# Performance work log

Measured on AMD Instinct MI355X. Metric: run time of the kernel, lower is better.

Reference implementation:

```python
import jax, jax.numpy as jnp
import numpy as np

N_NODES = 100000
N_EDGES = 1600000
NUM_FEATS = 128
HIDDEN = 16
NUM_CLASSES = 40


def setup_inputs() -> dict:
    key = jax.random.key(0)
    k1, k2, k3, k4, k5 = jax.random.split(key, 5)
    x = jax.random.normal(k1, (N_NODES, NUM_FEATS), dtype=jnp.float32)
    edge_weight = jax.random.uniform(k2, (N_EDGES,), dtype=jnp.float32)
    # Glorot-uniform linear weights (bias=False in the module)
    lim1 = float(np.sqrt(6.0 / (NUM_FEATS + HIDDEN)))
    lim2 = float(np.sqrt(6.0 / (HIDDEN + NUM_CLASSES)))
    W1 = jax.random.uniform(k3, (NUM_FEATS, HIDDEN), dtype=jnp.float32, minval=-lim1, maxval=lim1)
    W2 = jax.random.uniform(k4, (HIDDEN, NUM_CLASSES), dtype=jnp.float32, minval=-lim2, maxval=lim2)
    edge_index = jax.random.randint(k5, (2, N_EDGES), 0, N_NODES, dtype=jnp.int64)
    return {"x": x, "edge_weight": edge_weight, "W1": W1, "W2": W2, "edge_index": edge_index}


def _sgconv(h, W, src, dst, edge_weight, n):
    # SGConv (K=1): weighted neighbor aggregation + self loop (weight 1), then bias-free linear
    msg = edge_weight[:, None] * h[src]                      # [E, d] gather + scale
    agg = jax.ops.segment_sum(msg, dst, num_segments=n) + h  # scatter-add + self loop
    return agg @ W


def reference(x, edge_weight, W1, W2, edge_index):
    src, dst = edge_index[0], edge_index[1]
    n = x.shape[0]
    h = _sgconv(x, W1, src, dst, edge_weight, n)   # [N, 16]
    # dropout(p=0.5) is identity in eval mode
    h = _sgconv(h, W2, src, dst, edge_weight, n)   # [N, num_classes]
    return jax.nn.log_softmax(h, axis=1)
```

## Files before the change

### kernel.cpp

```cpp
#include <hip/hip_runtime.h>

#define NFEAT 128
#define HID 16
#define NCLS 40
#define BSHIFT 7
#define BNODES 128
#define CAP 2560
#define NBUCK_MAX 800
#define BIN_CHUNK 4096
#define APAD 17

#define SCALE1 262144.0f
#define SCALE2 65536.0f

typedef __attribute__((ext_vector_type(8))) short short8;
typedef __attribute__((ext_vector_type(4))) float f32x4;

__device__ __forceinline__ unsigned bf16_rne(float f) {
    unsigned u = __float_as_uint(f);
    return (u + 0x7FFFu + ((u >> 16) & 1u)) >> 16;
}
__device__ __forceinline__ float bf_lo(unsigned u) { return __uint_as_float(u << 16); }
__device__ __forceinline__ float bf_hi(unsigned u) { return __uint_as_float(u & 0xFFFF0000u); }

__global__ __launch_bounds__(256) void zero_kernel(int* __restrict__ p, int m)
{
    int i = blockIdx.x * 256 + threadIdx.x;
    if (i < m) p[i] = 0;
}

__global__ __launch_bounds__(256) void bin_kernel(const int* __restrict__ src,
                                                  const int* __restrict__ dst,
                                                  const float* __restrict__ ew,
                                                  int* __restrict__ cursor,
                                                  int2* __restrict__ slab,
                                                  int E, int nbuck)
{
    __shared__ int hist[NBUCK_MAX];
    __shared__ int runbase[NBUCK_MAX];
    __shared__ int lbase[NBUCK_MAX];
    __shared__ int2 ebuf[BIN_CHUNK];
    __shared__ unsigned short sbuck[BIN_CHUNK];
    __shared__ int sTotal;
    int tid = threadIdx.x;
    for (int i = tid; i < NBUCK_MAX; i += 256) hist[i] = 0;
    __syncthreads();

    int base = blockIdx.x * BIN_CHUNK;
    int myd[16], mys[16], myw[16];
    #pragma unroll
    for (int k = 0; k < 16; ++k) {
        int e = base + k * 256 + tid;
        if (e < E) {
            myd[k] = dst[e];
            mys[k] = src[e];
            myw[k] = __float_as_int(ew[e]);
            atomicAdd(&hist[myd[k] >> BSHIFT], 1);
        } else myd[k] = -1;
    }
    __syncthreads();

    for (int i = tid; i < nbuck; i += 256) {
        int c = hist[i];
        if (c) runbase[i] = i * CAP + atomicAdd(&cursor[i], c);
    }
    if (tid < 64) {
        int lane = tid;
        int carry = 0;
        for (int i0 = 0; i0 < NBUCK_MAX; i0 += 64) {
            int i = i0 + lane;
            int v = (i < NBUCK_MAX) ? hist[i] : 0;
            int incl = v;
            #pragma unroll
            for (int off = 1; off < 64; off <<= 1) {
                int t = __shfl_up(incl, off);
                if (lane >= off) incl += t;
            }
            if (i < NBUCK_MAX) lbase[i] = carry + incl - v;
            carry += __shfl(incl, 63);
        }
        if (lane == 0) sTotal = carry;
    }
    __syncthreads();

    for (int i = tid; i < NBUCK_MAX; i += 256) hist[i] = 0;
    __syncthreads();
    #pragma unroll
    for (int k = 0; k < 16; ++k) {
        int d = myd[k];
        if (d >= 0) {
            int b = d >> BSHIFT;
            int r = atomicAdd(&hist[b], 1);
            int j = lbase[b] + r;
            ebuf[j]  = make_int2(mys[k] | ((d & (BNODES - 1)) << 20), myw[k]);
            sbuck[j] = (unsigned short)b;
        }
    }
    __syncthreads();

    int totalv = sTotal;
    for (int j = tid; j < totalv; j += 256) {
        int b = sbuck[j];
        int pos = runbase[b] + (j - lbase[b]);
        if (pos < (b + 1) * CAP)
            slab[pos] = ebuf[j];
    }
}

__global__ __launch_bounds__(256) void gemm1_mfma_kernel(const float* __restrict__ x,
                                                         const float* __restrict__ W1,
                                                         unsigned short* __restrict__ h1b,
                                                         int n)
{
    int tid  = threadIdx.x;
    int wave = tid >> 6, lane = tid & 63;
    int m = lane & 15, q = lane >> 4;
    int base = blockIdx.x * 64 + wave * 16;

    short8 bfrag[4];
    #pragma unroll
    for (int kc = 0; kc < 4; ++kc) {
        #pragma unroll
        for (int j = 0; j < 8; ++j)
            bfrag[kc][j] = (short)bf16_rne(W1[(kc * 32 + q * 8 + j) * HID + m]);
    }

    int rowa = base + m; if (rowa > n - 1) rowa = n - 1;
    const float* xr = x + (size_t)rowa * NFEAT;
    f32x4 acc = {0.f, 0.f, 0.f, 0.f};
    #pragma unroll
    for (int kc = 0; kc < 4; ++kc) {
        float4 a0 = *(const float4*)(xr + kc * 32 + q * 8);
        float4 a1 = *(const float4*)(xr + kc * 32 + q * 8 + 4);
        short8 af;
        af[0] = (short)bf16_rne(a0.x); af[1] = (short)bf16_rne(a0.y);
        af[2] = (short)bf16_rne(a0.z); af[3] = (short)bf16_rne(a0.w);
        af[4] = (short)bf16_rne(a1.x); af[5] = (short)bf16_rne(a1.y);
        af[6] = (short)bf16_rne(a1.z); af[7] = (short)bf16_rne(a1.w);
        acc = __builtin_amdgcn_mfma_f32_16x16x32_bf16(af, bfrag[kc], acc, 0, 0, 0);
    }
    #pragma unroll
    for (int reg = 0; reg < 4; ++reg) {
        int rowd = base + q * 4 + reg;
        if (rowd < n)
            h1b[(size_t)rowd * HID + m] = (unsigned short)bf16_rne(acc[reg]);
    }
}

__global__ __launch_bounds__(512) void gather1_kernel(const uint4* __restrict__ hq,
                                                      const int* __restrict__ cursor,
                                                      const int2* __restrict__ slab,
                                                      uint4* __restrict__ outb, int n)
{
    __shared__ int accum[BNODES * APAD];
    int tid = threadIdx.x;
    #pragma unroll
    for (int i = tid; i < BNODES * APAD; i += 512) accum[i] = 0;
    __syncthreads();

    int b = blockIdx.x;
    int beg = b * CAP;
    int cnt = cursor[b]; if (cnt > CAP) cnt = CAP;
    int total = cnt * 2;

    int i0 = tid, i1 = tid + 512;
    int2 e0, e1; uint4 q0;
    if (i0 < total) e0 = slab[beg + (i0 >> 1)];
    if (i1 < total) e1 = slab[beg + (i1 >> 1)];
    if (i0 < total) q0 = hq[(size_t)(e0.x & 0xFFFFF) * 2 + (i0 & 1)];

    while (i0 < total) {
        uint4 q1;
        if (i1 < total) q1 = hq[(size_t)(e1.x & 0xFFFFF) * 2 + (i1 & 1)];
        int i2 = i1 + 512;
        int2 e2;
        if (i2 < total) e2 = slab[beg + (i2 >> 1)];

        int p  = i0 & 1;
        int dl = (e0.x >> 20) & (BNODES - 1);
        float wsc = __int_as_float(e0.y) * SCALE1;
        int* a = &accum[dl * APAD + p * 8];
        atomicAdd(a + 0, __float2int_rn(wsc * bf_lo(q0.x)));
        atomicAdd(a + 1, __float2int_rn(wsc * bf_hi(q0.x)));
        atomicAdd(a + 2, __float2int_rn(wsc * bf_lo(q0.y)));
        atomicAdd(a + 3, __float2int_rn(wsc * bf_hi(q0.y)));
        atomicAdd(a + 4, __float2int_rn(wsc * bf_lo(q0.z)));
        atomicAdd(a + 5, __float2int_rn(wsc * bf_hi(q0.z)));
        atomicAdd(a + 6, __float2int_rn(wsc * bf_lo(q0.w)));
        atomicAdd(a + 7, __float2int_rn(wsc * bf_hi(q0.w)));

        e0 = e1; e1 = e2; q0 = q1; i0 = i1; i1 = i2;
    }
    __syncthreads();

    const float inv = 1.0f / SCALE1;
    if (tid < BNODES * 2) {
        int dl = tid >> 1, p = tid & 1;
        int node = (b << BSHIFT) + dl;
        if (node < n) {
            uint4 qs = hq[(size_t)node * 2 + p];
            const int* a = &accum[dl * APAD + p * 8];
            uint4 o;
            o.x = bf16_rne((float)a[0] * inv + bf_lo(qs.x)) |
                  (bf16_rne((float)a[1] * inv + bf_hi(qs.x)) << 16);
            o.y = bf16_rne((float)a[2] * inv + bf_lo(qs.y)) |
                  (bf16_rne((float)a[3] * inv + bf_hi(qs.y)) << 16);
            o.z = bf16_rne((float)a[4] * inv + bf_lo(qs.z)) |
                  (bf16_rne((float)a[5] * inv + bf_hi(qs.z)) << 16);
            o.w = bf16_rne((float)a[6] * inv + bf_lo(qs.w)) |
                  (bf16_rne((float)a[7] * inv + bf_hi(qs.w)) << 16);
            outb[(size_t)node * 2 + p] = o;
        }
    }
}

#define ZPAD 41
__global__ __launch_bounds__(512) void gather2_lsm_kernel(const uint4* __restrict__ hq,
                                                          const int* __restrict__ cursor,
                                                          const int2* __restrict__ slab,
                                                          const float* __restrict__ W2,
                                                          float* __restrict__ out, int n)
{
    __shared__ int   accum[BNODES * APAD];
    __shared__ float w2s[HID * NCLS];
    __shared__ float zbuf[BNODES * ZPAD];
    int tid = threadIdx.x;
    #pragma unroll
    for (int i = tid; i < BNODES * APAD; i += 512) accum[i] = 0;
    for (int i = tid; i < HID * NCLS; i += 512) w2s[i] = W2[i];
    __syncthreads();

    int b = blockIdx.x;
    int beg = b * CAP;
    int cnt = cursor[b]; if (cnt > CAP) cnt = CAP;
    int node0 = b << BSHIFT;
    int total = cnt * 2;

    int i0 = tid, i1 = tid + 512;
    int2 e0, e1; uint4 q0;
    if (i0 < total) e0 = slab[beg + (i0 >> 1)];
    if (i1 < total) e1 = slab[beg + (i1 >> 1)];
    if (i0 < total) q0 = hq[(size_t)(e0.x & 0xFFFFF) * 2 + (i0 & 1)];

    while (i0 < total) {
        uint4 q1;
        if (i1 < total) q1 = hq[(size_t)(e1.x & 0xFFFFF) * 2 + (i1 & 1)];
        int i2 = i1 + 512;
        int2 e2;
        if (i2 < total) e2 = slab[beg + (i2 >> 1)];

        int p  = i0 & 1;
        int dl = (e0.x >> 20) & (BNODES - 1);
        float wsc = __int_as_float(e0.y) * SCALE2;
        int* a = &accum[dl * APAD + p * 8];
        atomicAdd(a + 0, __float2int_rn(wsc * bf_lo(q0.x)));
        atomicAdd(a + 1, __float2int_rn(wsc * bf_hi(q0.x)));
        atomicAdd(a + 2, __float2int_rn(wsc * bf_lo(q0.y)));
        atomicAdd(a + 3, __float2int_rn(wsc * bf_hi(q0.y)));
        atomicAdd(a + 4, __float2int_rn(wsc * bf_lo(q0.z)));
        atomicAdd(a + 5, __float2int_rn(wsc * bf_hi(q0.z)));
        atomicAdd(a + 6, __float2int_rn(wsc * bf_lo(q0.w)));
        atomicAdd(a + 7, __float2int_rn(wsc * bf_hi(q0.w)));

        e0 = e1; e1 = e2; q0 = q1; i0 = i1; i1 = i2;
    }
    __syncthreads();

    const float inv = 1.0f / SCALE2;
    if (tid < BNODES) {
        int dl = tid;
        int node = node0 + dl;
        if (node < n) {
            uint4 qa = hq[(size_t)node * 2 + 0];
            uint4 qb = hq[(size_t)node * 2 + 1];
            float r[HID];
            const int* a = &accum[dl * APAD];
            r[0]  = (float)a[ 0] * inv + bf_lo(qa.x);
            r[1]  = (float)a[ 1] * inv + bf_hi(qa.x);
            r[2]  = (float)a[ 2] * inv + bf_lo(qa.y);
            r[3]  = (float)a[ 3] * inv + bf_hi(qa.y);
            r[4]  = (float)a[ 4] * inv + bf_lo(qa.z);
            r[5]  = (float)a[ 5] * inv + bf_hi(qa.z);
            r[6]  = (float)a[ 6] * inv + bf_lo(qa.w);
            r[7]  = (float)a[ 7] * inv + bf_hi(qa.w);
            r[8]  = (float)a[ 8] * inv + bf_lo(qb.x);
            r[9]  = (float)a[ 9] * inv + bf_hi(qb.x);
            r[10] = (float)a[10] * inv + bf_lo(qb.y);
            r[11] = (float)a[11] * inv + bf_hi(qb.y);
            r[12] = (float)a[12] * inv + bf_lo(qb.z);
            r[13] = (float)a[13] * inv + bf_hi(qb.z);
            r[14] = (float)a[14] * inv + bf_lo(qb.w);
            r[15] = (float)a[15] * inv + bf_hi(qb.w);

            float z[NCLS];
            #pragma unroll
            for (int j = 0; j < NCLS; ++j) z[j] = 0.f;
            #pragma unroll
            for (int f = 0; f < HID; ++f) {
                float rf = r[f];
                #pragma unroll
                for (int j = 0; j < NCLS; ++j)
                    z[j] += rf * w2s[f * NCLS + j];
            }
            float m = z[0];
            #pragma unroll
            for (int j = 1; j < NCLS; ++j) m = fmaxf(m, z[j]);
            float ssum = 0.f;
            #pragma unroll
            for (int j = 0; j < NCLS; ++j) ssum += __expf(z[j] - m);
            float l = m + __logf(ssum);
            #pragma unroll
            for (int j = 0; j < NCLS; ++j) zbuf[dl * ZPAD + j] = z[j] - l;
        }
    }
    __syncthreads();

    for (int i = tid; i < BNODES * NCLS; i += 512) {
        int nl = i / NCLS, j = i - nl * NCLS;
        if (node0 + nl < n)
            out[(size_t)node0 * NCLS + i] = zbuf[nl * ZPAD + j];
    }
}

extern "C" void kernel_launch(void* const* d_in, const int* in_sizes, int n_in,
                              void* d_out, int out_size, void* d_ws, size_t ws_size,
                              hipStream_t stream)
{
    const float* x  = (const float*)d_in[0];
    const float* ew = (const float*)d_in[1];
    const float* W1 = (const float*)d_in[2];
    const float* W2 = (const float*)d_in[3];
    const int*   ei = (const int*)d_in[4];

    int n = in_sizes[0] / NFEAT;
    int E = in_sizes[1];
    const int* src = ei;
    const int* dst = ei + E;
    float* out = (float*)d_out;

    int nbuck = (n + BNODES - 1) >> BSHIFT;
    int nbin  = (E + BIN_CHUNK - 1) / BIN_CHUNK;

    char* w = (char*)d_ws;
    int*  cursor = (int*)w;  w += NBUCK_MAX * 4;
    w = (char*)(((size_t)w + 15) & ~(size_t)15);
    int2* slab   = (int2*)w; w += (size_t)NBUCK_MAX * CAP * 8;
    unsigned short* h1b = (unsigned short*)w; w += (size_t)n * HID * 2;
    unsigned short* h2b = (unsigned short*)w; w += (size_t)n * HID * 2;

    zero_kernel<<<(NBUCK_MAX + 255) / 256, 256, 0, stream>>>(cursor, NBUCK_MAX);
    bin_kernel<<<nbin, 256, 0, stream>>>(src, dst, ew, cursor, slab, E, nbuck);
    gemm1_mfma_kernel<<<(n + 63) / 64, 256, 0, stream>>>(x, W1, h1b, n);
    gather1_kernel<<<nbuck, 512, 0, stream>>>((const uint4*)h1b, cursor, slab,
                                              (uint4*)h2b, n);
    gather2_lsm_kernel<<<nbuck, 512, 0, stream>>>((const uint4*)h2b, cursor, slab,
                                                  W2, out, n);
}
```

Before: 171.9 us.

## Fuse whole pipeline into one cooperative persistent kernel with grid syncs

Replaces the five separate launches (zero, bin, gemm, gather1, gather2+log_softmax) with a single cooperative kernel of 256 persistent blocks that uses grid-wide syncs between phases. Binning and the first GEMM become one shared work queue, and binning now scatters straight to the slab without the local staging buffer or prefix scan. The aim is to remove launch gaps and tail effects between kernels. In exchange there are grid-sync costs, only 256 blocks covering about 800 buckets per gather phase, and less coalesced slab writes. If the cooperative launch fails, it falls back to a multi-kernel path that also fuses bin and GEMM.

```diff
diff --git a/kernel.cpp b/kernel.cpp
--- a/kernel.cpp
+++ b/kernel.cpp
@@ -1,4 +1,7 @@
 #include <hip/hip_runtime.h>
+#include <hip/hip_cooperative_groups.h>
+
+namespace cg = cooperative_groups;
 
 #define NFEAT 128
 #define HID 16
@@ -9,6 +12,7 @@
 #define NBUCK_MAX 800
 #define BIN_CHUNK 4096
 #define APAD 17
+#define ZPAD 41
 
 #define SCALE1 262144.0f
 #define SCALE2 65536.0f
@@ -22,6 +26,267 @@
 }
 __device__ __forceinline__ float bf_lo(unsigned u) { return __uint_as_float(u << 16); }
 __device__ __forceinline__ float bf_hi(unsigned u) { return __uint_as_float(u & 0xFFFF0000u); }
+
+__global__ __launch_bounds__(512, 2) void mega_kernel(
+    const int* __restrict__ src, const int* __restrict__ dst,
+    const float* __restrict__ ew, int* __restrict__ cursor,
+    int2* __restrict__ slab, int E, int nbuck, int nbin,
+    const float* __restrict__ x, const float* __restrict__ W1,
+    unsigned short* __restrict__ h1b, unsigned short* __restrict__ h2b,
+    const float* __restrict__ W2, float* __restrict__ out, int n)
+{
+    __shared__ int   hist[NBUCK_MAX];
+    __shared__ int   runbase[NBUCK_MAX];
+    __shared__ int   accum[BNODES * APAD];
+    __shared__ float w2s[HID * NCLS];
+    __shared__ float zbuf[BNODES * ZPAD];
+
+    cg::grid_group grid = cg::this_grid();
+    const int tid = threadIdx.x;
+    const int bid = blockIdx.x;
+    const int G   = gridDim.x;
+
+    for (int i = bid * 512 + tid; i < NBUCK_MAX; i += G * 512) cursor[i] = 0;
+    grid.sync();
+
+    int ngemm = (n + 127) >> 7;
+    int nunits = nbin + ngemm;
+    for (int u = bid; u < nunits; u += G) {
+        if (u < nbin) {
+            for (int i = tid; i < NBUCK_MAX; i += 512) hist[i] = 0;
+            __syncthreads();
+            int base = u * BIN_CHUNK;
+            int myd[8], mys[8], myw[8];
+            #pragma unroll
+            for (int k = 0; k < 8; ++k) {
+                int e = base + k * 512 + tid;
+                if (e < E) {
+                    myd[k] = dst[e];
+                    mys[k] = src[e];
+                    myw[k] = __float_as_int(ew[e]);
+                    atomicAdd(&hist[myd[k] >> BSHIFT], 1);
+                } else myd[k] = -1;
+            }
+            __syncthreads();
+            for (int i = tid; i < nbuck; i += 512) {
+                int c = hist[i];
+                runbase[i] = c ? (i * CAP + atomicAdd(&cursor[i], c)) : 0;
+                hist[i] = 0;
+            }
+            __syncthreads();
+            #pragma unroll
+            for (int k = 0; k < 8; ++k) {
+                int d = myd[k];
+                if (d >= 0) {
+                    int b = d >> BSHIFT;
+                    int pos = runbase[b] + atomicAdd(&hist[b], 1);
+                    if (pos < (b + 1) * CAP)
+                        slab[pos] = make_int2(mys[k] | ((d & (BNODES - 1)) << 20), myw[k]);
+                }
+            }
+            __syncthreads();
+        } else {
+            int wave = tid >> 6, lane = tid & 63;
+            int m = lane & 15, q = lane >> 4;
+            int rbase = (u - nbin) * 128 + wave * 16;
+
+            short8 bfrag[4];
+            #pragma unroll
+            for (int kc = 0; kc < 4; ++kc) {
+                #pragma unroll
+                for (int j = 0; j < 8; ++j)
+                    bfrag[kc][j] = (short)bf16_rne(W1[(kc * 32 + q * 8 + j) * HID + m]);
+            }
+            int rowa = rbase + m; if (rowa > n - 1) rowa = n - 1;
+            const float* xr = x + (size_t)rowa * NFEAT;
+            f32x4 acc = {0.f, 0.f, 0.f, 0.f};
+            #pragma unroll
+            for (int kc = 0; kc < 4; ++kc) {
+                float4 a0 = *(const float4*)(xr + kc * 32 + q * 8);
+                float4 a1 = *(const float4*)(xr + kc * 32 + q * 8 + 4);
+                short8 af;
+                af[0] = (short)bf16_rne(a0.x); af[1] = (short)bf16_rne(a0.y);
+                af[2] = (short)bf16_rne(a0.z); af[3] = (short)bf16_rne(a0.w);
+                af[4] = (short)bf16_rne(a1.x); af[5] = (short)bf16_rne(a1.y);
+                af[6] = (short)bf16_rne(a1.z); af[7] = (short)bf16_rne(a1.w);
+                acc = __builtin_amdgcn_mfma_f32_16x16x32_bf16(af, bfrag[kc], acc, 0, 0, 0);
+            }
+            #pragma unroll
+            for (int reg = 0; reg < 4; ++reg) {
+                int rowd = rbase + q * 4 + reg;
+                if (rowd < n)
+                    h1b[(size_t)rowd * HID + m] = (unsigned short)bf16_rne(acc[reg]);
+            }
+        }
+    }
+    grid.sync();
+
+    {
+        const uint4* hq = (const uint4*)h1b;
+        uint4* outb = (uint4*)h2b;
+        for (int b = bid; b < nbuck; b += G) {
+            for (int i = tid; i < BNODES * APAD; i += 512) accum[i] = 0;
+            __syncthreads();
+
+            int beg = b * CAP;
+            int cnt = cursor[b]; if (cnt > CAP) cnt = CAP;
+            int total = cnt * 2;
+
+            int i0 = tid, i1 = tid + 512;
+            int2 e0, e1; uint4 q0;
+            if (i0 < total) e0 = slab[beg + (i0 >> 1)];
+            if (i1 < total) e1 = slab[beg + (i1 >> 1)];
+            if (i0 < total) q0 = hq[(size_t)(e0.x & 0xFFFFF) * 2 + (i0 & 1)];
+
+            while (i0 < total) {
+                uint4 q1;
+                if (i1 < total) q1 = hq[(size_t)(e1.x & 0xFFFFF) * 2 + (i1 & 1)];
+                int i2 = i1 + 512;
+                int2 e2;
+                if (i2 < total) e2 = slab[beg + (i2 >> 1)];
+
+                int p  = i0 & 1;
+                int dl = (e0.x >> 20) & (BNODES - 1);
+                float wsc = __int_as_float(e0.y) * SCALE1;
+                int* a = &accum[dl * APAD + p * 8];
+                atomicAdd(a + 0, __float2int_rn(wsc * bf_lo(q0.x)));
+                atomicAdd(a + 1, __float2int_rn(wsc * bf_hi(q0.x)));
+                atomicAdd(a + 2, __float2int_rn(wsc * bf_lo(q0.y)));
+                atomicAdd(a + 3, __float2int_rn(wsc * bf_hi(q0.y)));
+                atomicAdd(a + 4, __float2int_rn(wsc * bf_lo(q0.z)));
+                atomicAdd(a + 5, __float2int_rn(wsc * bf_hi(q0.z)));
+                atomicAdd(a + 6, __float2int_rn(wsc * bf_lo(q0.w)));
+                atomicAdd(a + 7, __float2int_rn(wsc * bf_hi(q0.w)));
+
+                e0 = e1; e1 = e2; q0 = q1; i0 = i1; i1 = i2;
+            }
+            __syncthreads();
+
+            const float inv = 1.0f / SCALE1;
+            if (tid < BNODES * 2) {
+                int dl = tid >> 1, p = tid & 1;
+                int node = (b << BSHIFT) + dl;
+                if (node < n) {
+                    uint4 qs = hq[(size_t)node * 2 + p];
+                    const int* a = &accum[dl * APAD + p * 8];
+                    uint4 o;
+                    o.x = bf16_rne((float)a[0] * inv + bf_lo(qs.x)) |
+                          (bf16_rne((float)a[1] * inv + bf_hi(qs.x)) << 16);
+                    o.y = bf16_rne((float)a[2] * inv + bf_lo(qs.y)) |
+                          (bf16_rne((float)a[3] * inv + bf_hi(qs.y)) << 16);
+                    o.z = bf16_rne((float)a[4] * inv + bf_lo(qs.z)) |
+                          (bf16_rne((float)a[5] * inv + bf_hi(qs.z)) << 16);
+                    o.w = bf16_rne((float)a[6] * inv + bf_lo(qs.w)) |
+                          (bf16_rne((float)a[7] * inv + bf_hi(qs.w)) << 16);
+                    outb[(size_t)node * 2 + p] = o;
+                }
+            }
+            __syncthreads();
+        }
+    }
+    grid.sync();
+
+    {
+        const uint4* hq = (const uint4*)h2b;
+        for (int i = tid; i < HID * NCLS; i += 512) w2s[i] = W2[i];
+        for (int b = bid; b < nbuck; b += G) {
+            for (int i = tid; i < BNODES * APAD; i += 512) accum[i] = 0;
+            __syncthreads();
+
+            int beg = b * CAP;
+            int cnt = cursor[b]; if (cnt > CAP) cnt = CAP;
+            int node0 = b << BSHIFT;
+            int total = cnt * 2;
+
+            int i0 = tid, i1 = tid + 512;
+            int2 e0, e1; uint4 q0;
+            if (i0 < total) e0 = slab[beg + (i0 >> 1)];
+            if (i1 < total) e1 = slab[beg + (i1 >> 1)];
+            if (i0 < total) q0 = hq[(size_t)(e0.x & 0xFFFFF) * 2 + (i0 & 1)];
+
+            while (i0 < total) {
+                uint4 q1;
+                if (i1 < total) q1 = hq[(size_t)(e1.x & 0xFFFFF) * 2 + (i1 & 1)];
+                int i2 = i1 + 512;
+                int2 e2;
+                if (i2 < total) e2 = slab[beg + (i2 >> 1)];
+
+                int p  = i0 & 1;
+                int dl = (e0.x >> 20) & (BNODES - 1);
+                float wsc = __int_as_float(e0.y) * SCALE2;
+                int* a = &accum[dl * APAD + p * 8];
+                atomicAdd(a + 0, __float2int_rn(wsc * bf_lo(q0.x)));
+                atomicAdd(a + 1, __float2int_rn(wsc * bf_hi(q0.x)));
+                atomicAdd(a + 2, __float2int_rn(wsc * bf_lo(q0.y)));
+                atomicAdd(a + 3, __float2int_rn(wsc * bf_hi(q0.y)));
+                atomicAdd(a + 4, __float2int_rn(wsc * bf_lo(q0.z)));
+                atomicAdd(a + 5, __float2int_rn(wsc * bf_hi(q0.z)));
+                atomicAdd(a + 6, __float2int_rn(wsc * bf_lo(q0.w)));
+                atomicAdd(a + 7, __float2int_rn(wsc * bf_hi(q0.w)));
+
+                e0 = e1; e1 = e2; q0 = q1; i0 = i1; i1 = i2;
+            }
+            __syncthreads();
+
+            const float inv = 1.0f / SCALE2;
+            if (tid < BNODES) {
+                int dl = tid;
+                int node = node0 + dl;
+                if (node < n) {
+                    uint4 qa = hq[(size_t)node * 2 + 0];
+                    uint4 qb = hq[(size_t)node * 2 + 1];
+                    float r[HID];
+                    const int* a = &accum[dl * APAD];
+                    r[0]  = (float)a[ 0] * inv + bf_lo(qa.x);
+                    r[1]  = (float)a[ 1] * inv + bf_hi(qa.x);
+                    r[2]  = (float)a[ 2] * inv + bf_lo(qa.y);
+                    r[3]  = (float)a[ 3] * inv + bf_hi(qa.y);
+                    r[4]  = (float)a[ 4] * inv + bf_lo(qa.z);
+                    r[5]  = (float)a[ 5] * inv + bf_hi(qa.z);
+                    r[6]  = (float)a[ 6] * inv + bf_lo(qa.w);
+                    r[7]  = (float)a[ 7] * inv + bf_hi(qa.w);
+                    r[8]  = (float)a[ 8] * inv + bf_lo(qb.x);
+                    r[9]  = (float)a[ 9] * inv + bf_hi(qb.x);
+                    r[10] = (float)a[10] * inv + bf_lo(qb.y);
+                    r[11] = (float)a[11] * inv + bf_hi(qb.y);
+                    r[12] = (float)a[12] * inv + bf_lo(qb.z);
+                    r[13] = (float)a[13] * inv + bf_hi(qb.z);
+                    r[14] = (float)a[14] * inv + bf_lo(qb.w);
+                    r[15] = (float)a[15] * inv + bf_hi(qb.w);
+
+                    float z[NCLS];
+                    #pragma unroll
+                    for (int j = 0; j < NCLS; ++j) z[j] = 0.f;
+                    #pragma unroll
+                    for (int f = 0; f < HID; ++f) {
+                        float rf = r[f];
+                        #pragma unroll
+                        for (int j = 0; j < NCLS; ++j)
+                            z[j] += rf * w2s[f * NCLS + j];
+                    }
+                    float m = z[0];
+                    #pragma unroll
+                    for (int j = 1; j < NCLS; ++j) m = fmaxf(m, z[j]);
+                    float ssum = 0.f;
+                    #pragma unroll
+                    for (int j = 0; j < NCLS; ++j) ssum += __expf(z[j] - m);
+                    float l = m + __logf(ssum);
+                    #pragma unroll
+                    for (int j = 0; j < NCLS; ++j) zbuf[dl * ZPAD + j] = z[j] - l;
+                }
+            }
+            __syncthreads();
+
+            for (int i = tid; i < BNODES * NCLS; i += 512) {
+                int nl = i / NCLS, j = i - nl * NCLS;
+                if (node0 + nl < n)
+                    out[(size_t)node0 * NCLS + i] = zbuf[nl * ZPAD + j];
+            }
+            __syncthreads();
+        }
+    }
+}
+
 
 __global__ __launch_bounds__(256) void zero_kernel(int* __restrict__ p, int m)
 {
@@ -29,121 +294,87 @@
     if (i < m) p[i] = 0;
 }
 
-__global__ __launch_bounds__(256) void bin_kernel(const int* __restrict__ src,
-                                                  const int* __restrict__ dst,
-                                                  const float* __restrict__ ew,
-                                                  int* __restrict__ cursor,
-                                                  int2* __restrict__ slab,
-                                                  int E, int nbuck)
+__global__ __launch_bounds__(256) void bin_gemm_kernel(const int* __restrict__ src,
+                                                       const int* __restrict__ dst,
+                                                       const float* __restrict__ ew,
+                                                       int* __restrict__ cursor,
+                                                       int2* __restrict__ slab,
+                                                       int E, int nbuck, int nbin,
+                                                       const float* __restrict__ x,
+                                                       const float* __restrict__ W1,
+                                                       unsigned short* __restrict__ h1b,
+                                                       int n)
 {
     __shared__ int hist[NBUCK_MAX];
     __shared__ int runbase[NBUCK_MAX];
-    __shared__ int lbase[NBUCK_MAX];
-    __shared__ int2 ebuf[BIN_CHUNK];
-    __shared__ unsigned short sbuck[BIN_CHUNK];
-    __shared__ int sTotal;
     int tid = threadIdx.x;
-    for (int i = tid; i < NBUCK_MAX; i += 256) hist[i] = 0;
-    __syncthreads();
-
-    int base = blockIdx.x * BIN_CHUNK;
-    int myd[16], mys[16], myw[16];
-    #pragma unroll
-    for (int k = 0; k < 16; ++k) {
-        int e = base + k * 256 + tid;
-        if (e < E) {
-            myd[k] = dst[e];
-            mys[k] = src[e];
-            myw[k] = __float_as_int(ew[e]);
-            atomicAdd(&hist[myd[k] >> BSHIFT], 1);
-        } else myd[k] = -1;
-    }
-    __syncthreads();
-
-    for (int i = tid; i < nbuck; i += 256) {
-        int c = hist[i];
-        if (c) runbase[i] = i * CAP + atomicAdd(&cursor[i], c);
-    }
-    if (tid < 64) {
-        int lane = tid;
-        int carry = 0;
-        for (int i0 = 0; i0 < NBUCK_MAX; i0 += 64) {
-            int i = i0 + lane;
-            int v = (i < NBUCK_MAX) ? hist[i] : 0;
-            int incl = v;
-            #pragma unroll
-            for (int off = 1; off < 64; off <<= 1) {
-                int t = __shfl_up(incl, off);
-                if (lane >= off) incl += t;
-            }
-            if (i < NBUCK_MAX) lbase[i] = carry + incl - v;
-            carry += __shfl(incl, 63);
-        }
-        if (lane == 0) sTotal = carry;
-    }
-    __syncthreads();
-
-    for (int i = tid; i < NBUCK_MAX; i += 256) hist[i] = 0;
-    __syncthreads();
-    #pragma unroll
-    for (int k = 0; k < 16; ++k) {
-        int d = myd[k];
-        if (d >= 0) {
-            int b = d >> BSHIFT;
-            int r = atomicAdd(&hist[b], 1);
-            int j = lbase[b] + r;
-            ebuf[j]  = make_int2(mys[k] | ((d & (BNODES - 1)) << 20), myw[k]);
-            sbuck[j] = (unsigned short)b;
-        }
-    }
-    __syncthreads();
-
-    int totalv = sTotal;
-    for (int j = tid; j < totalv; j += 256) {
-        int b = sbuck[j];
-        int pos = runbase[b] + (j - lbase[b]);
-        if (pos < (b + 1) * CAP)
-            slab[pos] = ebuf[j];
-    }
-}
-
-__global__ __launch_bounds__(256) void gemm1_mfma_kernel(const float* __restrict__ x,
-                                                         const float* __restrict__ W1,
-                                                         unsigned short* __restrict__ h1b,
-                                                         int n)
-{
-    int tid  = threadIdx.x;
-    int wave = tid >> 6, lane = tid & 63;
-    int m = lane & 15, q = lane >> 4;
-    int base = blockIdx.x * 64 + wave * 16;
-
-    short8 bfrag[4];
-    #pragma unroll
-    for (int kc = 0; kc < 4; ++kc) {
+
+    if (blockIdx.x < nbin) {
+        for (int i = tid; i < NBUCK_MAX; i += 256) hist[i] = 0;
+        __syncthreads();
+
+        int base = blockIdx.x * BIN_CHUNK;
+        int myd[16], mys[16], myw[16];
         #pragma unroll
-        for (int j = 0; j < 8; ++j)
-            bfrag[kc][j] = (short)bf16_rne(W1[(kc * 32 + q * 8 + j) * HID + m]);
-    }
-
-    int rowa = base + m; if (rowa > n - 1) rowa = n - 1;
-    const float* xr = x + (size_t)rowa * NFEAT;
-    f32x4 acc = {0.f, 0.f, 0.f, 0.f};
-    #pragma unroll
-    for (int kc = 0; kc < 4; ++kc) {
-        float4 a0 = *(const float4*)(xr + kc * 32 + q * 8);
-        float4 a1 = *(const float4*)(xr + kc * 32 + q * 8 + 4);
-        short8 af;
-        af[0] = (short)bf16_rne(a0.x); af[1] = (short)bf16_rne(a0.y);
-        af[2] = (short)bf16_rne(a0.z); af[3] = (short)bf16_rne(a0.w);
-        af[4] = (short)bf16_rne(a1.x); af[5] = (short)bf16_rne(a1.y);
-        af[6] = (short)bf16_rne(a1.z); af[7] = (short)bf16_rne(a1.w);
-        acc = __builtin_amdgcn_mfma_f32_16x16x32_bf16(af, bfrag[kc], acc, 0, 0, 0);
-    }
-    #pragma unroll
-    for (int reg = 0; reg < 4; ++reg) {
-        int rowd = base + q * 4 + reg;
-        if (rowd < n)
-            h1b[(size_t)rowd * HID + m] = (unsigned short)bf16_rne(acc[reg]);
+        for (int k = 0; k < 16; ++k) {
+            int e = base + k * 256 + tid;
+            if (e < E) {
+                myd[k] = dst[e];
+                mys[k] = src[e];
+                myw[k] = __float_as_int(ew[e]);
+                atomicAdd(&hist[myd[k] >> BSHIFT], 1);
+            } else myd[k] = -1;
+        }
+        __syncthreads();
+        for (int i = tid; i < nbuck; i += 256) {
+            int c = hist[i];
+            runbase[i] = c ? (i * CAP + atomicAdd(&cursor[i], c)) : 0;
+            hist[i] = 0;
+        }
+        __syncthreads();
+        #pragma unroll
+        for (int k = 0; k < 16; ++k) {
+            int d = myd[k];
+            if (d >= 0) {
+                int b = d >> BSHIFT;
+                int pos = runbase[b] + atomicAdd(&hist[b], 1);
+                if (pos < (b + 1) * CAP)
+                    slab[pos] = make_int2(mys[k] | ((d & (BNODES - 1)) << 20), myw[k]);
+            }
+        }
+    } else {
+        int wave = tid >> 6, lane = tid & 63;
+        int m = lane & 15, q = lane >> 4;
+        int base = (blockIdx.x - nbin) * 64 + wave * 16;
+
+        short8 bfrag[4];
+        #pragma unroll
+        for (int kc = 0; kc < 4; ++kc) {
+            #pragma unroll
+            for (int j = 0; j < 8; ++j)
+                bfrag[kc][j] = (short)bf16_rne(W1[(kc * 32 + q * 8 + j) * HID + m]);
+        }
+
+        int rowa = base + m; if (rowa > n - 1) rowa = n - 1;
+        const float* xr = x + (size_t)rowa * NFEAT;
+        f32x4 acc = {0.f, 0.f, 0.f, 0.f};
+        #pragma unroll
+        for (int kc = 0; kc < 4; ++kc) {
+            float4 a0 = *(const float4*)(xr + kc * 32 + q * 8);
+            float4 a1 = *(const float4*)(xr + kc * 32 + q * 8 + 4);
+            short8 af;
+            af[0] = (short)bf16_rne(a0.x); af[1] = (short)bf16_rne(a0.y);
+            af[2] = (short)bf16_rne(a0.z); af[3] = (short)bf16_rne(a0.w);
+            af[4] = (short)bf16_rne(a1.x); af[5] = (short)bf16_rne(a1.y);
+            af[6] = (short)bf16_rne(a1.z); af[7] = (short)bf16_rne(a1.w);
+            acc = __builtin_amdgcn_mfma_f32_16x16x32_bf16(af, bfrag[kc], acc, 0, 0, 0);
+        }
+        #pragma unroll
+        for (int reg = 0; reg < 4; ++reg) {
+            int rowd = base + q * 4 + reg;
+            if (rowd < n)
+                h1b[(size_t)rowd * HID + m] = (unsigned short)bf16_rne(acc[reg]);
+        }
     }
 }
 
@@ -214,7 +445,6 @@
     }
 }
 
-#define ZPAD 41
 __global__ __launch_bounds__(512) void gather2_lsm_kernel(const uint4* __restrict__ hq,
                                                           const int* __restrict__ cursor,
                                                           const int2* __restrict__ slab,
@@ -348,11 +578,21 @@
     unsigned short* h1b = (unsigned short*)w; w += (size_t)n * HID * 2;
     unsigned short* h2b = (unsigned short*)w; w += (size_t)n * HID * 2;
 
-    zero_kernel<<<(NBUCK_MAX + 255) / 256, 256, 0, stream>>>(cursor, NBUCK_MAX);
-    bin_kernel<<<nbin, 256, 0, stream>>>(src, dst, ew, cursor, slab, E, nbuck);
-    gemm1_mfma_kernel<<<(n + 63) / 64, 256, 0, stream>>>(x, W1, h1b, n);
-    gather1_kernel<<<nbuck, 512, 0, stream>>>((const uint4*)h1b, cursor, slab,
-                                              (uint4*)h2b, n);
-    gather2_lsm_kernel<<<nbuck, 512, 0, stream>>>((const uint4*)h2b, cursor, slab,
-                                                  W2, out, n);
-}
+    void* kargs[] = {
+        (void*)&src, (void*)&dst, (void*)&ew, (void*)&cursor, (void*)&slab,
+        (void*)&E, (void*)&nbuck, (void*)&nbin, (void*)&x, (void*)&W1,
+        (void*)&h1b, (void*)&h2b, (void*)&W2, (void*)&out, (void*)&n
+    };
+    hipError_t err = hipLaunchCooperativeKernel((void*)mega_kernel, dim3(256),
+                                                dim3(512), kargs, 0, stream);
+    if (err != hipSuccess) {
+        int ngemm64 = (n + 63) / 64;
+        zero_kernel<<<(NBUCK_MAX + 255) / 256, 256, 0, stream>>>(cursor, NBUCK_MAX);
+        bin_gemm_kernel<<<nbin + ngemm64, 256, 0, stream>>>(src, dst, ew, cursor, slab,
+                                                            E, nbuck, nbin, x, W1, h1b, n);
+        gather1_kernel<<<nbuck, 512, 0, stream>>>((const uint4*)h1b, cursor, slab,
+                                                  (uint4*)h2b, n);
+        gather2_lsm_kernel<<<nbuck, 512, 0, stream>>>((const uint4*)h2b, cursor, slab,
+                                                      W2, out, n);
+    }
+}
```

After: 268.0 us. +55.9%, slower.

## Merge binning and GEMM1 into one launch, deepen gather prefetch pipelines

Applied to the files above, without the earlier changes.

Binning and the first MFMA GEMM now run as disjoint block ranges of a single kernel, so the two independent stages overlap and one launch is saved. The binning path drops the LDS staging buffer and prefix scan and scatters each edge straight to its global slab slot. This reduces LDS use, which may raise occupancy, but the global writes are less coalesced. Both gather kernels prefetch four edges and three feature rows ahead instead of two and one, and carry occupancy hints in their launch bounds, trading registers for more memory-level parallelism.

```diff
diff --git a/kernel.cpp b/kernel.cpp
--- a/kernel.cpp
+++ b/kernel.cpp
@@ -9,6 +9,7 @@
 #define NBUCK_MAX 800
 #define BIN_CHUNK 4096
 #define APAD 17
+#define ZPAD 41
 
 #define SCALE1 262144.0f
 #define SCALE2 65536.0f
@@ -29,128 +30,94 @@
     if (i < m) p[i] = 0;
 }
 
-__global__ __launch_bounds__(256) void bin_kernel(const int* __restrict__ src,
-                                                  const int* __restrict__ dst,
-                                                  const float* __restrict__ ew,
-                                                  int* __restrict__ cursor,
-                                                  int2* __restrict__ slab,
-                                                  int E, int nbuck)
+__global__ __launch_bounds__(256) void bin_gemm_kernel(const int* __restrict__ src,
+                                                       const int* __restrict__ dst,
+                                                       const float* __restrict__ ew,
+                                                       int* __restrict__ cursor,
+                                                       int2* __restrict__ slab,
+                                                       int E, int nbuck, int nbin,
+                                                       const float* __restrict__ x,
+                                                       const float* __restrict__ W1,
+                                                       unsigned short* __restrict__ h1b,
+                                                       int n)
 {
     __shared__ int hist[NBUCK_MAX];
     __shared__ int runbase[NBUCK_MAX];
-    __shared__ int lbase[NBUCK_MAX];
-    __shared__ int2 ebuf[BIN_CHUNK];
-    __shared__ unsigned short sbuck[BIN_CHUNK];
-    __shared__ int sTotal;
     int tid = threadIdx.x;
-    for (int i = tid; i < NBUCK_MAX; i += 256) hist[i] = 0;
-    __syncthreads();
-
-    int base = blockIdx.x * BIN_CHUNK;
-    int myd[16], mys[16], myw[16];
-    #pragma unroll
-    for (int k = 0; k < 16; ++k) {
-        int e = base + k * 256 + tid;
-        if (e < E) {
-            myd[k] = dst[e];
-            mys[k] = src[e];
-            myw[k] = __float_as_int(ew[e]);
-            atomicAdd(&hist[myd[k] >> BSHIFT], 1);
-        } else myd[k] = -1;
-    }
-    __syncthreads();
-
-    for (int i = tid; i < nbuck; i += 256) {
-        int c = hist[i];
-        if (c) runbase[i] = i * CAP + atomicAdd(&cursor[i], c);
-    }
-    if (tid < 64) {
-        int lane = tid;
-        int carry = 0;
-        for (int i0 = 0; i0 < NBUCK_MAX; i0 += 64) {
-            int i = i0 + lane;
-            int v = (i < NBUCK_MAX) ? hist[i] : 0;
-            int incl = v;
-            #pragma unroll
-            for (int off = 1; off < 64; off <<= 1) {
-                int t = __shfl_up(incl, off);
-                if (lane >= off) incl += t;
+
+    if (blockIdx.x < nbin) {
+        for (int i = tid; i < NBUCK_MAX; i += 256) hist[i] = 0;
+        __syncthreads();
+
+        int base = blockIdx.x * BIN_CHUNK;
+        int myd[16], mys[16], myw[16];
+        #pragma unroll
+        for (int k = 0; k < 16; ++k) {
+            int e = base + k * 256 + tid;
+            if (e < E) {
+                myd[k] = dst[e];
+                mys[k] = src[e];
+                myw[k] = __float_as_int(ew[e]);
+                atomicAdd(&hist[myd[k] >> BSHIFT], 1);
+            } else myd[k] = -1;
+        }
+        __syncthreads();
+        for (int i = tid; i < nbuck; i += 256) {
+            int c = hist[i];
+            runbase[i] = c ? (i * CAP + atomicAdd(&cursor[i], c)) : 0;
+            hist[i] = 0;
+        }
+        __syncthreads();
+        #pragma unroll
+        for (int k = 0; k < 16; ++k) {
+            int d = myd[k];
+            if (d >= 0) {
+                int b = d >> BSHIFT;
+                int pos = runbase[b] + atomicAdd(&hist[b], 1);
+                if (pos < (b + 1) * CAP)
+                    slab[pos] = make_int2(mys[k] | ((d & (BNODES - 1)) << 20), myw[k]);
             }
-            if (i < NBUCK_MAX) lbase[i] = carry + incl - v;
-            carry += __shfl(incl, 63);
-        }
-        if (lane == 0) sTotal = carry;
-    }
-    __syncthreads();
-
-    for (int i = tid; i < NBUCK_MAX; i += 256) hist[i] = 0;
-    __syncthreads();
-    #pragma unroll
-    for (int k = 0; k < 16; ++k) {
-        int d = myd[k];
-        if (d >= 0) {
-            int b = d >> BSHIFT;
-            int r = atomicAdd(&hist[b], 1);
-            int j = lbase[b] + r;
-            ebuf[j]  = make_int2(mys[k] | ((d & (BNODES - 1)) << 20), myw[k]);
-            sbuck[j] = (unsigned short)b;
-        }
-    }
-    __syncthreads();
-
-    int totalv = sTotal;
-    for (int j = tid; j < totalv; j += 256) {
-        int b = sbuck[j];
-        int pos = runbase[b] + (j - lbase[b]);
-        if (pos < (b + 1) * CAP)
-            slab[pos] = ebuf[j];
-    }
-}
-
-__global__ __launch_bounds__(256) void gemm1_mfma_kernel(const float* __restrict__ x,
-                                                         const float* __restrict__ W1,
-                                                         unsigned short* __restrict__ h1b,
-                                                         int n)
-{
-    int tid  = threadIdx.x;
-    int wave = tid >> 6, lane = tid & 63;
-    int m = lane & 15, q = lane >> 4;
-    int base = blockIdx.x * 64 + wave * 16;
-
-    short8 bfrag[4];
-    #pragma unroll
-    for (int kc = 0; kc < 4; ++kc) {
-        #pragma unroll
-        for (int j = 0; j < 8; ++j)
-            bfrag[kc][j] = (short)bf16_rne(W1[(kc * 32 + q * 8 + j) * HID + m]);
-    }
-
-    int rowa = base + m; if (rowa > n - 1) rowa = n - 1;
-    const float* xr = x + (size_t)rowa * NFEAT;
-    f32x4 acc = {0.f, 0.f, 0.f, 0.f};
-    #pragma unroll
-    for (int kc = 0; kc < 4; ++kc) {
-        float4 a0 = *(const float4*)(xr + kc * 32 + q * 8);
-        float4 a1 = *(const float4*)(xr + kc * 32 + q * 8 + 4);
-        short8 af;
-        af[0] = (short)bf16_rne(a0.x); af[1] = (short)bf16_rne(a0.y);
-        af[2] = (short)bf16_rne(a0.z); af[3] = (short)bf16_rne(a0.w);
-        af[4] = (short)bf16_rne(a1.x); af[5] = (short)bf16_rne(a1.y);
-        af[6] = (short)bf16_rne(a1.z); af[7] = (short)bf16_rne(a1.w);
-        acc = __builtin_amdgcn_mfma_f32_16x16x32_bf16(af, bfrag[kc], acc, 0, 0, 0);
-    }
-    #pragma unroll
-    for (int reg = 0; reg < 4; ++reg) {
-        int rowd = base + q * 4 + reg;
-        if (rowd < n)
-            h1b[(size_t)rowd * HID + m] = (unsigned short)bf16_rne(acc[reg]);
-    }
-}
-
-__global__ __launch_bounds__(512) void gather1_kernel(const uint4* __restrict__ hq,
-                                                      const int* __restrict__ cursor,
-                                                      const int2* __restrict__ slab,
-                                                      uint4* __restrict__ outb, int n)
+        }
+    } else {
+        int wave = tid >> 6, lane = tid & 63;
+        int m = lane & 15, q = lane >> 4;
+        int base = (blockIdx.x - nbin) * 64 + wave * 16;
+
+        short8 bfrag[4];
+        #pragma unroll
+        for (int kc = 0; kc < 4; ++kc) {
+            #pragma unroll
+            for (int j = 0; j < 8; ++j)
+                bfrag[kc][j] = (short)bf16_rne(W1[(kc * 32 + q * 8 + j) * HID + m]);
+        }
+
+        int rowa = base + m; if (rowa > n - 1) rowa = n - 1;
+        const float* xr = x + (size_t)rowa * NFEAT;
+        f32x4 acc = {0.f, 0.f, 0.f, 0.f};
+        #pragma unroll
+        for (int kc = 0; kc < 4; ++kc) {
+            float4 a0 = *(const float4*)(xr + kc * 32 + q * 8);
+            float4 a1 = *(const float4*)(xr + kc * 32 + q * 8 + 4);
+            short8 af;
+            af[0] = (short)bf16_rne(a0.x); af[1] = (short)bf16_rne(a0.y);
+            af[2] = (short)bf16_rne(a0.z); af[3] = (short)bf16_rne(a0.w);
+            af[4] = (short)bf16_rne(a1.x); af[5] = (short)bf16_rne(a1.y);
+            af[6] = (short)bf16_rne(a1.z); af[7] = (short)bf16_rne(a1.w);
+            acc = __builtin_amdgcn_mfma_f32_16x16x32_bf16(af, bfrag[kc], acc, 0, 0, 0);
+        }
+        #pragma unroll
+        for (int reg = 0; reg < 4; ++reg) {
+            int rowd = base + q * 4 + reg;
+            if (rowd < n)
+                h1b[(size_t)rowd * HID + m] = (unsigned short)bf16_rne(acc[reg]);
+        }
+    }
+}
+
+__global__ __launch_bounds__(512, 8) void gather1_kernel(const uint4* __restrict__ hq,
+                                                         const int* __restrict__ cursor,
+                                                         const int2* __restrict__ slab,
+                                                         uint4* __restrict__ outb, int n)
 {
     __shared__ int accum[BNODES * APAD];
     int tid = threadIdx.x;
@@ -163,18 +130,22 @@
     int cnt = cursor[b]; if (cnt > CAP) cnt = CAP;
     int total = cnt * 2;
 
-    int i0 = tid, i1 = tid + 512;
-    int2 e0, e1; uint4 q0;
+    int i0 = tid, i1 = tid + 512, i2 = tid + 1024, i3 = tid + 1536;
+    int2 e0, e1, e2, e3; uint4 q0, q1, q2;
     if (i0 < total) e0 = slab[beg + (i0 >> 1)];
     if (i1 < total) e1 = slab[beg + (i1 >> 1)];
+    if (i2 < total) e2 = slab[beg + (i2 >> 1)];
+    if (i3 < total) e3 = slab[beg + (i3 >> 1)];
     if (i0 < total) q0 = hq[(size_t)(e0.x & 0xFFFFF) * 2 + (i0 & 1)];
+    if (i1 < total) q1 = hq[(size_t)(e1.x & 0xFFFFF) * 2 + (i1 & 1)];
+    if (i2 < total) q2 = hq[(size_t)(e2.x & 0xFFFFF) * 2 + (i2 & 1)];
 
     while (i0 < total) {
-        uint4 q1;
-        if (i1 < total) q1 = hq[(size_t)(e1.x & 0xFFFFF) * 2 + (i1 & 1)];
-        int i2 = i1 + 512;
-        int2 e2;
-        if (i2 < total) e2 = slab[beg + (i2 >> 1)];
+        uint4 q3;
+        if (i3 < total) q3 = hq[(size_t)(e3.x & 0xFFFFF) * 2 + (i3 & 1)];
+        int i4 = i3 + 512;
+        int2 e4;
+        if (i4 < total) e4 = slab[beg + (i4 >> 1)];
 
         int p  = i0 & 1;
         int dl = (e0.x >> 20) & (BNODES - 1);
@@ -189,7 +160,9 @@
         atomicAdd(a + 6, __float2int_rn(wsc * bf_lo(q0.w)));
         atomicAdd(a + 7, __float2int_rn(wsc * bf_hi(q0.w)));
 
-        e0 = e1; e1 = e2; q0 = q1; i0 = i1; i1 = i2;
+        e0 = e1; e1 = e2; e2 = e3; e3 = e4;
+        q0 = q1; q1 = q2; q2 = q3;
+        i0 = i1; i1 = i2; i2 = i3; i3 = i4;
     }
     __syncthreads();
 
@@ -214,12 +187,11 @@
     }
 }
 
-#define ZPAD 41
-__global__ __launch_bounds__(512) void gather2_lsm_kernel(const uint4* __restrict__ hq,
-                                                          const int* __restrict__ cursor,
-                                                          const int2* __restrict__ slab,
-                                                          const float* __restrict__ W2,
-                                                          float* __restrict__ out, int n)
+__global__ __launch_bounds__(512, 6) void gather2_lsm_kernel(const uint4* __restrict__ hq,
+                                                             const int* __restrict__ cursor,
+                                                             const int2* __restrict__ slab,
+                                                             const float* __restrict__ W2,
+                                                             float* __restrict__ out, int n)
 {
     __shared__ int   accum[BNODES * APAD];
     __shared__ float w2s[HID * NCLS];
@@ -236,18 +208,22 @@
     int node0 = b << BSHIFT;
     int total = cnt * 2;
 
-    int i0 = tid, i1 = tid + 512;
-    int2 e0, e1; uint4 q0;
+    int i0 = tid, i1 = tid + 512, i2 = tid + 1024, i3 = tid + 1536;
+    int2 e0, e1, e2, e3; uint4 q0, q1, q2;
     if (i0 < total) e0 = slab[beg + (i0 >> 1)];
     if (i1 < total) e1 = slab[beg + (i1 >> 1)];
+    if (i2 < total) e2 = slab[beg + (i2 >> 1)];
+    if (i3 < total) e3 = slab[beg + (i3 >> 1)];
     if (i0 < total) q0 = hq[(size_t)(e0.x & 0xFFFFF) * 2 + (i0 & 1)];
+    if (i1 < total) q1 = hq[(size_t)(e1.x & 0xFFFFF) * 2 + (i1 & 1)];
+    if (i2 < total) q2 = hq[(size_t)(e2.x & 0xFFFFF) * 2 + (i2 & 1)];
 
     while (i0 < total) {
-        uint4 q1;
-        if (i1 < total) q1 = hq[(size_t)(e1.x & 0xFFFFF) * 2 + (i1 & 1)];
-        int i2 = i1 + 512;
-        int2 e2;
-        if (i2 < total) e2 = slab[beg + (i2 >> 1)];
+        uint4 q3;
+        if (i3 < total) q3 = hq[(size_t)(e3.x & 0xFFFFF) * 2 + (i3 & 1)];
+        int i4 = i3 + 512;
+        int2 e4;
+        if (i4 < total) e4 = slab[beg + (i4 >> 1)];
 
         int p  = i0 & 1;
         int dl = (e0.x >> 20) & (BNODES - 1);
@@ -262,7 +238,9 @@
         atomicAdd(a + 6, __float2int_rn(wsc * bf_lo(q0.w)));
         atomicAdd(a + 7, __float2int_rn(wsc * bf_hi(q0.w)));
 
-        e0 = e1; e1 = e2; q0 = q1; i0 = i1; i1 = i2;
+        e0 = e1; e1 = e2; e2 = e3; e3 = e4;
+        q0 = q1; q1 = q2; q2 = q3;
+        i0 = i1; i1 = i2; i2 = i3; i3 = i4;
     }
     __syncthreads();
 
@@ -340,6 +318,7 @@
 
     int nbuck = (n + BNODES - 1) >> BSHIFT;
     int nbin  = (E + BIN_CHUNK - 1) / BIN_CHUNK;
+    int ngemm = (n + 63) / 64;
 
     char* w = (char*)d_ws;
     int*  cursor = (int*)w;  w += NBUCK_MAX * 4;
@@ -349,8 +328,8 @@
     unsigned short* h2b = (unsigned short*)w; w += (size_t)n * HID * 2;
 
     zero_kernel<<<(NBUCK_MAX + 255) / 256, 256, 0, stream>>>(cursor, NBUCK_MAX);
-    bin_kernel<<<nbin, 256, 0, stream>>>(src, dst, ew, cursor, slab, E, nbuck);
-    gemm1_mfma_kernel<<<(n + 63) / 64, 256, 0, stream>>>(x, W1, h1b, n);
+    bin_gemm_kernel<<<nbin + ngemm, 256, 0, stream>>>(src, dst, ew, cursor, slab,
+                                                      E, nbuck, nbin, x, W1, h1b, n);
     gather1_kernel<<<nbuck, 512, 0, stream>>>((const uint4*)h1b, cursor, slab,
                                               (uint4*)h2b, n);
     gather2_lsm_kernel<<<nbuck, 512, 0, stream>>>((const uint4*)h2b, cursor, slab,
```

Measured after the change: 169.0 us. About the same (-1.7%).
